# Performance work log

Hardware: AMD Instinct MI355X
Metric: run time of the kernel (lower is better)

## Reference

```python
import jax, jax.numpy as jnp
import numpy as np

D_MODEL = 512
B, T = 4, 4096


def setup_inputs() -> dict:
    key = jax.random.key(0)
    k1, k2, k3 = jax.random.split(key, 3)
    x = jax.random.normal(k1, (B, T, D_MODEL), dtype=jnp.float32)
    # torch nn.Linear weight layout: [out_features, in_features]
    w_qkv = jax.random.normal(k2, (3 * D_MODEL, D_MODEL), dtype=jnp.float32) * (1.0 / np.sqrt(D_MODEL))
    w_proj = jax.random.normal(k3, (D_MODEL, D_MODEL), dtype=jnp.float32) * (1.0 / np.sqrt(D_MODEL))
    return {"x": x, "w_qkv": w_qkv, "w_proj": w_proj}


def reference(x, w_qkv, w_proj):
    # Faithful to the torch module: NO head split; attention over full d_model.
    Bx, Tx, C = x.shape
    qkv = jnp.einsum('btc,oc->bto', x, w_qkv)  # [B,T,3C]
    q, k, v = jnp.split(qkv, 3, axis=-1)
    scale = 1.0 / jnp.sqrt(jnp.asarray(C, x.dtype))
    scores = jnp.einsum('btc,bsc->bts', q, k) * scale  # [B,T,T]
    causal = jnp.tril(jnp.ones((Tx, Tx), dtype=bool))
    scores = jnp.where(causal[None, :, :], scores, -jnp.inf)
    weights = jax.nn.softmax(scores, axis=-1)
    out = jnp.einsum('bts,bsc->btc', weights, v)
    return jnp.einsum('btc,oc->bto', out, w_proj)
```

## Files before the change

### kernel.cpp

```cpp
#include <hip/hip_runtime.h>
#include <hip/hip_bf16.h>
#include <stdint.h>

typedef __bf16 bf16_t;
typedef __bf16 bf16x4 __attribute__((ext_vector_type(4)));
typedef __bf16 bf16x8 __attribute__((ext_vector_type(8)));
typedef short s16x4 __attribute__((ext_vector_type(4)));
typedef float f32x4 __attribute__((ext_vector_type(4)));

static_assert(sizeof(bf16x8) == 16, "bf16x8 must be 16B");

#define MFMA_BF16(a, b, c) __builtin_amdgcn_mfma_f32_16x16x32_bf16((a), (b), (c), 0, 0, 0)

__device__ __forceinline__ f32x4 mfma16(bf16x4 a, bf16x4 b, f32x4 c) {
#if __has_builtin(__builtin_amdgcn_mfma_f32_16x16x16bf16_1k)
  union { bf16x4 h; s16x4 s; } ua, ub;
  ua.h = a;
  ub.h = b;
  return __builtin_amdgcn_mfma_f32_16x16x16bf16_1k(ua.s, ub.s, c, 0, 0, 0);
#else
  f32x4 d = c;
  asm volatile("v_mfma_f32_16x16x16_bf16 %0, %1, %2, %0" : "+v"(d) : "v"(a), "v"(b));
  return d;
#endif
}

typedef const __attribute__((address_space(1))) void* gas_ptr;
typedef __attribute__((address_space(3))) void* las_ptr;

__device__ __forceinline__ void gload_lds16(const void* g, void* l) {
  __builtin_amdgcn_global_load_lds((gas_ptr)g, (las_ptr)l, 16, 0, 0);
}

#define NEG_BIG (-1.0e30f)

__global__ __launch_bounds__(256) void cvt_kernel(const float* __restrict__ src,
                                                  bf16_t* __restrict__ dst) {
  const int i = (blockIdx.x * 256 + threadIdx.x) * 4;
  const f32x4 v = *(const f32x4*)(src + i);
  bf16x4 o;
  o[0] = (bf16_t)v[0];
  o[1] = (bf16_t)v[1];
  o[2] = (bf16_t)v[2];
  o[3] = (bf16_t)v[3];
  *(bf16x4*)(dst + i) = o;
}

template <int MODE>
__global__ __launch_bounds__(256, 2) void gemm_bt_kernel(
    const bf16_t* __restrict__ A, const bf16_t* __restrict__ Bw,
    bf16_t* __restrict__ o_q, bf16_t* __restrict__ o_k, bf16_t* __restrict__ o_vT,
    float* __restrict__ o_f) {
  constexpr int K = 512;
  __shared__ bf16_t As[128 * 32];
  __shared__ bf16_t Bs[128 * 32];

  const int tid = threadIdx.x;
  const int lane = tid & 63;
  const int wid = tid >> 6;
  const int quad = lane >> 4;
  const int l15 = lane & 15;
  const int wm = wid >> 1;
  const int wn = wid & 1;

  const int mt = blockIdx.x & 127;
  const int nt = blockIdx.x >> 7;
  const int row0 = mt * 128;
  const int col0 = nt * 128;

  f32x4 acc[4][4] = {};

  for (int kt = 0; kt < K; kt += 32) {
    __syncthreads();
#pragma unroll
    for (int rnd = 0; rnd < 2; rnd++) {
      const int e = (rnd * 256 + tid) * 8;
      const int r = e >> 5;
      const int c = e & 31;
      gload_lds16(A + (size_t)(row0 + r) * K + kt + c, As + e);
      gload_lds16(Bw + (size_t)(col0 + r) * K + kt + c, Bs + e);
    }
    __syncthreads();

    bf16x8 af[4], bfr[4];
#pragma unroll
    for (int i = 0; i < 4; i++)
      af[i] = *(const bf16x8*)(As + (wm * 64 + i * 16 + l15) * 32 + quad * 8);
#pragma unroll
    for (int i = 0; i < 4; i++)
      bfr[i] = *(const bf16x8*)(Bs + (wn * 64 + i * 16 + l15) * 32 + quad * 8);
#pragma unroll
    for (int mi = 0; mi < 4; mi++)
#pragma unroll
      for (int ni = 0; ni < 4; ni++)
        acc[mi][ni] = MFMA_BF16(af[mi], bfr[ni], acc[mi][ni]);
  }

#pragma unroll
  for (int mi = 0; mi < 4; mi++) {
    const int row = row0 + wm * 64 + mi * 16 + quad * 4;
#pragma unroll
    for (int ni = 0; ni < 4; ni++) {
      const int col = col0 + wn * 64 + ni * 16 + l15;
#pragma unroll
      for (int r = 0; r < 4; r++) {
        const int rr = row + r;
        if constexpr (MODE == 0) {
          const bf16_t bv = (bf16_t)acc[mi][ni][r];
          if (col < 512) {
            o_q[(size_t)rr * 512 + col] = bv;
          } else if (col < 1024) {
            o_k[(size_t)rr * 512 + (col - 512)] = bv;
          } else {
            const int bb = rr >> 12;
            const int t = rr & 4095;
            o_vT[((size_t)bb * 512 + (col - 1024)) * 4096 + t] = bv;
          }
        } else {
          o_f[(size_t)rr * 512 + col] = acc[mi][ni][r];
        }
      }
    }
  }
}

__global__ __launch_bounds__(256, 2) void attn_part_kernel(
    const bf16_t* __restrict__ q, const bf16_t* __restrict__ k,
    const bf16_t* __restrict__ vT, bf16_t* __restrict__ partO,
    float2* __restrict__ stats) {
  __shared__ bf16_t SB[16384];

  const int tid = threadIdx.x;
  const int lane = tid & 63;
  const int wid = tid >> 6;
  const int quad = lane >> 4;
  const int l15 = lane & 15;

  const int bid = blockIdx.x;
  const int b = bid & 3;
  const int w = bid >> 2;
  int g = 0;
  while (w >= 4 * (g + 1) * (g + 2)) g++;
  const int rem = w - 4 * g * (g + 1);
  const int i = rem / (g + 1);
  const int c = rem - i * (g + 1);
  const int s = 8 * g + i;

  const int t0w = s * 64 + wid * 16;
  const int kv0 = c * 512;
  const int mmax = min(31, (t0w + 15 - kv0) >> 4);
  const int kvtmax = mmax >> 2;

  const float scale = 0.044194173824159216f;
  const bf16_t* kbase = k + ((size_t)b * 4096 + kv0) * 512;

  bf16x8 qf[16];
  {
    const bf16_t* qp = q + ((size_t)(b * 4096 + t0w + l15)) * 512 + quad * 8;
#pragma unroll
    for (int kk = 0; kk < 16; kk++) qf[kk] = *(const bf16x8*)(qp + kk * 32);
  }

  f32x4 Sacc[32];
#pragma unroll
  for (int m = 0; m < 32; m++) Sacc[m] = f32x4{0.f, 0.f, 0.f, 0.f};

  const int abase =
      ((l15 >> 2) * 16 + (quad ^ ((l15 >> 2) & 3)) * 4 + (l15 & 3)) * 8;

#pragma unroll
  for (int kt = 0; kt < 16; kt++) {
    __syncthreads();
#pragma unroll
    for (int rnd = 0; rnd < 8; rnd++) {
      const int ch = rnd * 256 + tid;
      const int g4 = ch >> 4;
      const int w16 = ch & 15;
      const int cg = (w16 >> 2) ^ (g4 & 3);
      const int row = g4 * 4 + (w16 & 3);
      gload_lds16(kbase + (size_t)row * 512 + kt * 32 + cg * 8, SB + ch * 8);
    }
    __syncthreads();
#pragma unroll
    for (int m = 0; m < 32; m++) {
      if (m <= mmax) {
        const bf16x8 kf = *(const bf16x8*)(SB + abase + m * 512);
        Sacc[m] = MFMA_BF16(kf, qf[kt], Sacc[m]);
      }
    }
  }

  const int qr = t0w + l15;
  float mx = NEG_BIG;
#pragma unroll
  for (int m = 0; m < 32; m++) {
    if (m <= mmax) {
#pragma unroll
      for (int r = 0; r < 4; r++) {
        const int kv = kv0 + m * 16 + quad * 4 + r;
        const float vvv = (kv <= qr) ? Sacc[m][r] : NEG_BIG;
        Sacc[m][r] = vvv;
        mx = fmaxf(mx, vvv);
      }
    }
  }
  mx = fmaxf(mx, __shfl_xor(mx, 16));
  mx = fmaxf(mx, __shfl_xor(mx, 32));

  float lrow = 0.0f;
  bf16x4 pb[32];
#pragma unroll
  for (int m = 0; m < 32; m++) {
    bf16x4 pv = {};
    if (m <= mmax) {
#pragma unroll
      for (int r = 0; r < 4; r++) {
        const float p = __expf((Sacc[m][r] - mx) * scale);
        pv[r] = (bf16_t)p;
        lrow += p;
      }
    }
    pb[m] = pv;
  }
  lrow += __shfl_xor(lrow, 16);
  lrow += __shfl_xor(lrow, 32);

  if (quad == 0)
    stats[((size_t)w * 4 + b) * 64 + wid * 16 + l15] =
        make_float2(mx * scale, lrow);

  const int l64 = l15 * 64;
  const int qh = quad >> 1;
  const int ql = (quad & 1) * 4;
  const int s7 = l15 & 7;

  for (int dh = 0; dh < 2; dh++) {
    const bf16_t* vbase = vT + ((size_t)(b * 512 + dh * 256)) * 4096 + kv0;
    f32x4 Oacc[16];
#pragma unroll
    for (int dt = 0; dt < 16; dt++) Oacc[dt] = f32x4{0.f, 0.f, 0.f, 0.f};

#pragma unroll
    for (int kvt = 0; kvt < 8; kvt++) {
      __syncthreads();
#pragma unroll
      for (int rnd = 0; rnd < 8; rnd++) {
        const int ch = rnd * 256 + tid;
        const int d = ch >> 3;
        const int cg = (ch & 7) ^ (d & 7);
        gload_lds16(vbase + (size_t)d * 4096 + kvt * 64 + cg * 8, SB + ch * 8);
      }
      __syncthreads();
      if (kvt <= kvtmax) {
#pragma unroll
        for (int dt = 0; dt < 16; dt++) {
#pragma unroll
          for (int gg = 0; gg < 4; gg++) {
            const bf16x4 vf = *(const bf16x4*)(
                SB + dt * 1024 + l64 + (((gg * 2 + qh) ^ s7) << 3) + ql);
            Oacc[dt] = mfma16(pb[kvt * 4 + gg], vf, Oacc[dt]);
          }
        }
      }
    }

    bf16_t* pbase = partO + (size_t)bid * 32768 + dh * 256;
#pragma unroll
    for (int rr = 0; rr < 4; rr++) {
      bf16_t* prow = pbase + (size_t)(wid * 16 + quad * 4 + rr) * 512 + l15;
#pragma unroll
      for (int dt = 0; dt < 16; dt++) prow[dt * 16] = (bf16_t)Oacc[dt][rr];
    }
  }
}

__global__ __launch_bounds__(256) void attn_combine_kernel(
    const bf16_t* __restrict__ partO, const float2* __restrict__ stats,
    bf16_t* __restrict__ o) {
  const int b = blockIdx.x & 3;
  const int s = blockIdx.x >> 2;
  const int g = s >> 3;
  const int nc = g + 1;
  const int w0 = 4 * g * (g + 1) + (s & 7) * (g + 1);

  __shared__ float wgt[8][64];
  __shared__ float linv[64];

  const int tid = threadIdx.x;
  if (tid < 64) {
    float mc[8], lc[8];
    float M = NEG_BIG;
    for (int cc = 0; cc < nc; cc++) {
      const float2 ml = stats[((size_t)(w0 + cc) * 4 + b) * 64 + tid];
      mc[cc] = ml.x;
      lc[cc] = ml.y;
      M = fmaxf(M, ml.x);
    }
    float L = 0.0f;
    for (int cc = 0; cc < nc; cc++) {
      const float wv = __expf(mc[cc] - M);
      wgt[cc][tid] = wv;
      L += wv * lc[cc];
    }
    linv[tid] = (L > 0.0f) ? 1.0f / L : 0.0f;
  }
  __syncthreads();

#pragma unroll
  for (int it = 0; it < 16; it++) {
    const int idx = it * 256 + tid;
    const int row = idx >> 6;
    const int d8 = (idx & 63) * 8;
    float acc[8] = {};
    for (int cc = 0; cc < nc; cc++) {
      const int bidc = ((w0 + cc) << 2) | b;
      const bf16x8 p = *(const bf16x8*)(partO + (size_t)bidc * 32768 +
                                        (size_t)row * 512 + d8);
      const float wv = wgt[cc][row];
#pragma unroll
      for (int e = 0; e < 8; e++) acc[e] += wv * (float)p[e];
    }
    const float li = linv[row];
    bf16x8 ov;
#pragma unroll
    for (int e = 0; e < 8; e++) ov[e] = (bf16_t)(acc[e] * li);
    *(bf16x8*)(o + ((size_t)(b * 4096 + s * 64 + row)) * 512 + d8) = ov;
  }
}

extern "C" void kernel_launch(void* const* d_in, const int* in_sizes, int n_in,
                              void* d_out, int out_size, void* d_ws, size_t ws_size,
                              hipStream_t stream) {
  const float* x_f = (const float*)d_in[0];
  const float* wq_f = (const float*)d_in[1];
  const float* wp_f = (const float*)d_in[2];
  float* out = (float*)d_out;

  bf16_t* xb = (bf16_t*)d_ws;
  bf16_t* wqb = xb + (size_t)16384 * 512;
  bf16_t* wpb = wqb + (size_t)1536 * 512;
  bf16_t* q = wpb + (size_t)512 * 512;
  bf16_t* kk = q + (size_t)16384 * 512;
  bf16_t* vT = kk + (size_t)16384 * 512;
  bf16_t* partO = vT + (size_t)16384 * 512;
  float2* stats = (float2*)(partO + (size_t)1152 * 32768);

  cvt_kernel<<<(16384 * 512) / 1024, 256, 0, stream>>>(x_f, xb);
  cvt_kernel<<<(1536 * 512) / 1024, 256, 0, stream>>>(wq_f, wqb);
  cvt_kernel<<<(512 * 512) / 1024, 256, 0, stream>>>(wp_f, wpb);

  gemm_bt_kernel<0><<<128 * 12, 256, 0, stream>>>(xb, wqb, q, kk, vT, nullptr);
  attn_part_kernel<<<1152, 256, 0, stream>>>(q, kk, vT, partO, stats);
  attn_combine_kernel<<<256, 256, 0, stream>>>(partO, stats, xb);
  gemm_bt_kernel<1><<<128 * 4, 256, 0, stream>>>(xb, wpb, nullptr, nullptr, nullptr, out);
}
```

Before: 411.6 us.

## Double-buffer K/V LDS staging and skip fully masked tiles in attention

Doubles the shared-memory buffer so the next K or V tile is prefetched into LDS while MFMAs run on the current one, removing one barrier per tile and chaining the K phase into the first V tile. It also limits K staging rounds and V tile loops to the block-level causal extent, skipping loads and iterations for fully masked key tiles. It adds s_setprio around the MFMA sections. The cost is twice the LDS per block (64 KB), which may lower occupancy below the two blocks per CU requested by the launch bounds.

```diff
diff --git a/kernel.cpp b/kernel.cpp
--- a/kernel.cpp
+++ b/kernel.cpp
@@ -128,7 +128,7 @@
     const bf16_t* __restrict__ q, const bf16_t* __restrict__ k,
     const bf16_t* __restrict__ vT, bf16_t* __restrict__ partO,
     float2* __restrict__ stats) {
-  __shared__ bf16_t SB[16384];
+  __shared__ bf16_t SB[2][16384];
 
   const int tid = threadIdx.x;
   const int lane = tid & 63;
@@ -150,44 +150,73 @@
   const int kv0 = c * 512;
   const int mmax = min(31, (t0w + 15 - kv0) >> 4);
   const int kvtmax = mmax >> 2;
+  const int mmax_blk = min(31, (s * 64 + 63 - kv0) >> 4);
+  const int kvtmax_blk = mmax_blk >> 2;
 
   const float scale = 0.044194173824159216f;
   const bf16_t* kbase = k + ((size_t)b * 4096 + kv0) * 512;
-
-  bf16x8 qf[16];
-  {
-    const bf16_t* qp = q + ((size_t)(b * 4096 + t0w + l15)) * 512 + quad * 8;
-#pragma unroll
-    for (int kk = 0; kk < 16; kk++) qf[kk] = *(const bf16x8*)(qp + kk * 32);
-  }
-
-  f32x4 Sacc[32];
-#pragma unroll
-  for (int m = 0; m < 32; m++) Sacc[m] = f32x4{0.f, 0.f, 0.f, 0.f};
-
-  const int abase =
-      ((l15 >> 2) * 16 + (quad ^ ((l15 >> 2) & 3)) * 4 + (l15 & 3)) * 8;
-
-#pragma unroll
-  for (int kt = 0; kt < 16; kt++) {
-    __syncthreads();
-#pragma unroll
-    for (int rnd = 0; rnd < 8; rnd++) {
+  const bf16_t* vbase = vT + ((size_t)b * 512) * 4096 + kv0;
+
+  auto stageK = [&](int kt, int buf) {
+    for (int rnd = 0; rnd <= kvtmax_blk; rnd++) {
       const int ch = rnd * 256 + tid;
       const int g4 = ch >> 4;
       const int w16 = ch & 15;
       const int cg = (w16 >> 2) ^ (g4 & 3);
       const int row = g4 * 4 + (w16 & 3);
-      gload_lds16(kbase + (size_t)row * 512 + kt * 32 + cg * 8, SB + ch * 8);
-    }
-    __syncthreads();
+      gload_lds16(kbase + (size_t)row * 512 + kt * 32 + cg * 8,
+                  &SB[buf][ch * 8]);
+    }
+  };
+  auto stageV = [&](int dh, int kvt, int buf) {
+    const bf16_t* vb = vbase + (size_t)(dh * 256) * 4096;
+#pragma unroll
+    for (int rnd = 0; rnd < 8; rnd++) {
+      const int ch = rnd * 256 + tid;
+      const int d = ch >> 3;
+      const int cg = (ch & 7) ^ (d & 7);
+      gload_lds16(vb + (size_t)d * 4096 + kvt * 64 + cg * 8, &SB[buf][ch * 8]);
+    }
+  };
+
+  stageK(0, 0);
+
+  bf16x8 qf[16];
+  {
+    const bf16_t* qp = q + ((size_t)(b * 4096 + t0w + l15)) * 512 + quad * 8;
+#pragma unroll
+    for (int kk = 0; kk < 16; kk++) qf[kk] = *(const bf16x8*)(qp + kk * 32);
+  }
+
+  f32x4 Sacc[32];
+#pragma unroll
+  for (int m = 0; m < 32; m++) Sacc[m] = f32x4{0.f, 0.f, 0.f, 0.f};
+
+  const int abase =
+      ((l15 >> 2) * 16 + (quad ^ ((l15 >> 2) & 3)) * 4 + (l15 & 3)) * 8;
+
+  __syncthreads();
+
+  int cur = 0;
+#pragma unroll
+  for (int kt = 0; kt < 16; kt++) {
+    if (kt < 15)
+      stageK(kt + 1, cur ^ 1);
+    else
+      stageV(0, 0, cur ^ 1);
+
+    const bf16_t* sb = &SB[cur][0];
+    __builtin_amdgcn_s_setprio(1);
 #pragma unroll
     for (int m = 0; m < 32; m++) {
       if (m <= mmax) {
-        const bf16x8 kf = *(const bf16x8*)(SB + abase + m * 512);
+        const bf16x8 kf = *(const bf16x8*)(sb + abase + m * 512);
         Sacc[m] = MFMA_BF16(kf, qf[kt], Sacc[m]);
       }
     }
+    __builtin_amdgcn_s_setprio(0);
+    __syncthreads();
+    cur ^= 1;
   }
 
   const int qr = t0w + l15;
@@ -235,33 +264,32 @@
   const int s7 = l15 & 7;
 
   for (int dh = 0; dh < 2; dh++) {
-    const bf16_t* vbase = vT + ((size_t)(b * 512 + dh * 256)) * 4096 + kv0;
     f32x4 Oacc[16];
 #pragma unroll
     for (int dt = 0; dt < 16; dt++) Oacc[dt] = f32x4{0.f, 0.f, 0.f, 0.f};
 
-#pragma unroll
-    for (int kvt = 0; kvt < 8; kvt++) {
-      __syncthreads();
-#pragma unroll
-      for (int rnd = 0; rnd < 8; rnd++) {
-        const int ch = rnd * 256 + tid;
-        const int d = ch >> 3;
-        const int cg = (ch & 7) ^ (d & 7);
-        gload_lds16(vbase + (size_t)d * 4096 + kvt * 64 + cg * 8, SB + ch * 8);
-      }
-      __syncthreads();
+    for (int kvt = 0; kvt <= kvtmax_blk; kvt++) {
+      if (kvt < kvtmax_blk)
+        stageV(dh, kvt + 1, cur ^ 1);
+      else if (dh == 0)
+        stageV(1, 0, cur ^ 1);
+
       if (kvt <= kvtmax) {
+        const bf16_t* sb = &SB[cur][0];
+        __builtin_amdgcn_s_setprio(1);
 #pragma unroll
         for (int dt = 0; dt < 16; dt++) {
 #pragma unroll
           for (int gg = 0; gg < 4; gg++) {
             const bf16x4 vf = *(const bf16x4*)(
-                SB + dt * 1024 + l64 + (((gg * 2 + qh) ^ s7) << 3) + ql);
+                sb + dt * 1024 + l64 + (((gg * 2 + qh) ^ s7) << 3) + ql);
             Oacc[dt] = mfma16(pb[kvt * 4 + gg], vf, Oacc[dt]);
           }
         }
-      }
+        __builtin_amdgcn_s_setprio(0);
+      }
+      __syncthreads();
+      cur ^= 1;
     }
 
     bf16_t* pbase = partO + (size_t)bid * 32768 + dh * 256;
```

Result: slower. 422.1 us (+2.5%).
